# Kernel optimization log

Measured on AMD Instinct MI355X. Metric: run time of the kernel, lower is better.

The kernel has to match this reference:

```python
import jax, jax.numpy as jnp
import numpy as np

DIM = 4096
N_HEADS = 32
HEAD_DIM = DIM // N_HEADS  # 128
B = 2
S = 2048
ADAPTER_LEN = 10
NEG_INF = -1e30


def _rope(t, cos, sin):
    # t: [B, S, H, hd]; cos/sin: [S, hd//2]
    b, s, h, d = t.shape
    tr = t.reshape(b, s, h, d // 2, 2)
    a, bb = tr[..., 0], tr[..., 1]
    c = cos[None, :, None, :]
    sn = sin[None, :, None, :]
    out = jnp.stack([a * c - bb * sn, a * sn + bb * c], axis=-1)
    return out.reshape(b, s, h, d)


def _attn(q, k, v, mask=None):
    # q: [B,H,Q,d], k/v: [B,H,K,d]
    scores = jnp.einsum('bhqd,bhkd->bhqk', q, k) / np.sqrt(HEAD_DIM).astype(q.dtype)
    if mask is not None:
        scores = scores + mask
    probs = jax.nn.softmax(scores.astype(jnp.float32), axis=-1).astype(q.dtype)
    return jnp.einsum('bhqk,bhkd->bhqd', probs, v)


def setup_inputs() -> dict:
    key = jax.random.key(0)
    ks = jax.random.split(key, 8)
    w_std = 0.02
    x = jax.random.normal(ks[0], (B, S, DIM), dtype=jnp.float32)
    wq = jax.random.normal(ks[1], (DIM, DIM), dtype=jnp.float32) * w_std
    wk = jax.random.normal(ks[2], (DIM, DIM), dtype=jnp.float32) * w_std
    wv = jax.random.normal(ks[3], (DIM, DIM), dtype=jnp.float32) * w_std
    wo = jax.random.normal(ks[4], (DIM, DIM), dtype=jnp.float32) * w_std
    gate = jax.random.normal(ks[5], (1, N_HEADS, 1, 1), dtype=jnp.float32)
    adapter = jax.random.normal(ks[6], (1, ADAPTER_LEN, DIM), dtype=jnp.float32)
    # RoPE tables (theta = 10000)
    inv_freq = 1.0 / (10000.0 ** (np.arange(0, HEAD_DIM, 2, dtype=np.float32) / HEAD_DIM))
    angles = np.outer(np.arange(S, dtype=np.float32), inv_freq)  # [S, hd//2]
    freqs_cos = jnp.asarray(np.cos(angles), dtype=jnp.float32)
    freqs_sin = jnp.asarray(np.sin(angles), dtype=jnp.float32)
    # causal additive mask [1,1,S,S]
    mask = jnp.triu(jnp.full((S, S), NEG_INF, dtype=jnp.float32), k=1)[None, None]
    return {"x": x, "wq": wq, "wk": wk, "wv": wv, "wo": wo, "gate": gate,
            "adapter": adapter, "freqs_cos": freqs_cos, "freqs_sin": freqs_sin,
            "mask": mask, "start_pos": 0}


def reference(x, wq, wk, wv, wo, gate, adapter, freqs_cos, freqs_sin, mask, start_pos):
    bsz, seqlen, _ = x.shape
    # QKV projections (torch Linear: y = x @ W.T)
    xq = jnp.einsum('bsd,ed->bse', x, wq).reshape(bsz, seqlen, N_HEADS, HEAD_DIM)
    xk = jnp.einsum('bsd,ed->bse', x, wk).reshape(bsz, seqlen, N_HEADS, HEAD_DIM)
    xv = jnp.einsum('bsd,ed->bse', x, wv).reshape(bsz, seqlen, N_HEADS, HEAD_DIM)
    xq = _rope(xq, freqs_cos, freqs_sin)
    xk = _rope(xk, freqs_cos, freqs_sin)
    # KV-cache write + read: start_pos == 0 and cache is zero-initialized, so
    # keys/values over [:start_pos+seqlen] equal the freshly written xk/xv.
    q = xq.transpose(0, 2, 1, 3)      # [B,H,S,d]
    keys = xk.transpose(0, 2, 1, 3)
    values = xv.transpose(0, 2, 1, 3)
    output = _attn(q, keys, values, mask)
    # gated adapter cross-attention
    a_k = jnp.einsum('bld,ed->ble', adapter, wk).reshape(1, ADAPTER_LEN, N_HEADS, HEAD_DIM)
    a_v = jnp.einsum('bld,ed->ble', adapter, wv).reshape(1, ADAPTER_LEN, N_HEADS, HEAD_DIM)
    a_k = jnp.broadcast_to(a_k, (bsz, ADAPTER_LEN, N_HEADS, HEAD_DIM)).transpose(0, 2, 1, 3)
    a_v = jnp.broadcast_to(a_v, (bsz, ADAPTER_LEN, N_HEADS, HEAD_DIM)).transpose(0, 2, 1, 3)
    output = output + jnp.tanh(gate) * _attn(q, a_k, a_v)
    output = output.transpose(0, 2, 1, 3).reshape(bsz, seqlen, DIM)
    return jnp.einsum('bse,de->bsd', output, wo)
```

## Files before the change

### kernel.cpp

```cpp
#include <hip/hip_runtime.h>

typedef unsigned short u16;
typedef __attribute__((ext_vector_type(8))) short short8;
typedef __attribute__((ext_vector_type(4))) float f32x4;

#define L2E   1.44269504088896340736f
#define SCALE 0.08838834764831845f
#define NEGI  -1e30f
#define WN    ((size_t)4096 * 4096)
#define TNB   ((size_t)2048 * 4096)

__device__ __forceinline__ float b2f(u16 u) {
  union { float f; unsigned int i; } v; v.i = ((unsigned int)u) << 16; return v.f;
}
__device__ __forceinline__ u16 f2b(float f) {
  union { float f; unsigned int i; } v; v.f = f;
  unsigned int r = v.i + 0x7fffu + ((v.i >> 16) & 1u);
  return (u16)(r >> 16);
}
__device__ __forceinline__ void gload16(const u16* g, u16* l) {
  __builtin_amdgcn_global_load_lds((const __attribute__((address_space(1))) void*)g,
                                   (__attribute__((address_space(3))) void*)l, 16, 0, 0);
}
__device__ __forceinline__ short8 ld8_f32_to_bf16(const float* p) {
  float4 a = *(const float4*)p;
  float4 b = *(const float4*)(p + 4);
  short8 pk;
  pk[0] = (short)f2b(a.x); pk[1] = (short)f2b(a.y);
  pk[2] = (short)f2b(a.z); pk[3] = (short)f2b(a.w);
  pk[4] = (short)f2b(b.x); pk[5] = (short)f2b(b.y);
  pk[6] = (short)f2b(b.z); pk[7] = (short)f2b(b.w);
  return pk;
}

__global__ __launch_bounds__(256) void cvt_bf16(const float* __restrict__ src,
                                                u16* __restrict__ dst)
{
  size_t e = ((size_t)blockIdx.x * 256 + threadIdx.x) * 8;
  *(short8*)(dst + e) = ld8_f32_to_bf16(src + e);
}

__global__ __launch_bounds__(256, 2) void gemm_nt(const u16* __restrict__ A,
    const u16* __restrict__ B, void* __restrict__ Cv, int mode)
{
  __shared__ __align__(16) u16 As[128 * 64];
  __shared__ __align__(16) u16 Bs[128 * 64];
  const int tid  = threadIdx.x;
  const int wave = tid >> 6, lane = tid & 63;
  const int quad = lane >> 4, l16 = lane & 15;
  const int bm = blockIdx.y * 128, bn = blockIdx.x * 128;
  const int wm = (wave >> 1) * 64, wn = (wave & 1) * 64;

  f32x4 acc[4][4];
#pragma unroll
  for (int i = 0; i < 4; i++)
#pragma unroll
    for (int j = 0; j < 4; j++) acc[i][j] = (f32x4)0.0f;

  for (int k0 = 0; k0 < 4096; k0 += 64) {
    __syncthreads();
#pragma unroll
    for (int i = 0; i < 4; i++) {
      int c = tid + i * 256;
      int row = c >> 3, cb = (c & 7) << 3;
      gload16(A + (((size_t)(bm + row)) << 12) + k0 + cb, As + c * 8);
      gload16(B + (((size_t)(bn + row)) << 12) + k0 + cb, Bs + c * 8);
    }
    __syncthreads();
#pragma unroll
    for (int ks = 0; ks < 2; ks++) {
      short8 af[4], bf[4];
#pragma unroll
      for (int t = 0; t < 4; t++) {
        af[t] = *(const short8*)(As + (wm + t * 16 + l16) * 64 + ks * 32 + quad * 8);
        bf[t] = *(const short8*)(Bs + (wn + t * 16 + l16) * 64 + ks * 32 + quad * 8);
      }
#pragma unroll
      for (int mt = 0; mt < 4; mt++)
#pragma unroll
        for (int nt = 0; nt < 4; nt++)
          acc[mt][nt] = __builtin_amdgcn_mfma_f32_16x16x32_bf16(af[mt], bf[nt], acc[mt][nt], 0, 0, 0);
    }
  }
#pragma unroll
  for (int mt = 0; mt < 4; mt++)
#pragma unroll
    for (int nt = 0; nt < 4; nt++)
#pragma unroll
      for (int r = 0; r < 4; r++) {
        int row = bm + wm + mt * 16 + quad * 4 + r;
        int col = bn + wn + nt * 16 + l16;
        float v = acc[mt][nt][r];
        if (mode == 2) {
          ((float*)Cv)[(((size_t)row) << 12) + col] = v;
        } else if (mode == 1) {
          ((u16*)Cv)[((size_t)(row >> 11)) * TNB + (((size_t)col) << 11) + (row & 2047)] = f2b(v);
        } else {
          ((u16*)Cv)[(((size_t)row) << 12) + col] = f2b(v);
        }
      }
}

__global__ __launch_bounds__(256) void rope_kernel(u16* __restrict__ Q, u16* __restrict__ K,
    const float* __restrict__ fc, const float* __restrict__ fs)
{
  int gid = blockIdx.x * 256 + threadIdx.x;
  int tsel = gid >> 21;
  int r = gid & 2097151;
  int row = r >> 9, gp = r & 511;
  int s = row & 2047;
  int e0 = gp * 8;
  int i0 = (e0 >> 1) & 63;
  u16* p = (tsel ? K : Q) + (((size_t)row) << 12) + e0;
  short8 v = *(const short8*)p;
  float4 c4 = *(const float4*)(fc + s * 64 + i0);
  float4 s4 = *(const float4*)(fs + s * 64 + i0);
  float cc[4] = {c4.x, c4.y, c4.z, c4.w};
  float ss[4] = {s4.x, s4.y, s4.z, s4.w};
  short8 w;
#pragma unroll
  for (int j = 0; j < 4; j++) {
    float a  = b2f((u16)v[2 * j]);
    float bb = b2f((u16)v[2 * j + 1]);
    w[2 * j]     = (short)f2b(a * cc[j] - bb * ss[j]);
    w[2 * j + 1] = (short)f2b(a * ss[j] + bb * cc[j]);
  }
  *(short8*)p = w;
}

__global__ __launch_bounds__(256) void adapter_kv(const float* __restrict__ adapter,
    const float* __restrict__ wk, const float* __restrict__ wv,
    u16* __restrict__ ak, u16* __restrict__ av)
{
  int gid  = blockIdx.x * 4 + (threadIdx.x >> 6);
  int lane = threadIdx.x & 63;
  int which = (gid >= 40960) ? 1 : 0;
  int rem = gid - which * 40960;
  int l = rem >> 12, col = rem & 4095;
  const float* w = which ? wv : wk;
  u16* o = which ? av : ak;
  const float* arow = adapter + l * 4096;
  const float* wrow = w + (((size_t)col) << 12);
  float sum = 0.f;
#pragma unroll
  for (int i = 0; i < 8; i++) {
    int e = i * 512 + lane * 8;
    float4 a0 = *(const float4*)(arow + e);
    float4 a1 = *(const float4*)(arow + e + 4);
    float4 w0 = *(const float4*)(wrow + e);
    float4 w1 = *(const float4*)(wrow + e + 4);
    sum += a0.x * w0.x + a0.y * w0.y + a0.z * w0.z + a0.w * w0.w
         + a1.x * w1.x + a1.y * w1.y + a1.z * w1.z + a1.w * w1.w;
  }
#pragma unroll
  for (int off = 1; off < 64; off <<= 1) sum += __shfl_xor(sum, off, 64);
  if (lane == 0) o[rem] = f2b(sum);
}

__global__ __launch_bounds__(256, 2) void flash_attn(const u16* __restrict__ Q,
    const u16* __restrict__ K, const u16* __restrict__ V, u16* __restrict__ O)
{
  Q += (size_t)blockIdx.z * TNB;
  K += (size_t)blockIdx.z * TNB;
  V += (size_t)blockIdx.z * TNB;
  O += (size_t)blockIdx.z * TNB;
  __shared__ __align__(16) u16 sm[24576];
  u16* Ks = sm;
  u16* Vs = sm + 8192;
  u16* Ps = sm + 16384;
  const int tid  = threadIdx.x;
  const int wave = tid >> 6, lane = tid & 63;
  const int quad = lane >> 4, l16 = lane & 15;
  const int qt = blockIdx.x;
  const int h  = blockIdx.y;
  const int q0 = qt * 128;
  const size_t qkBase = (size_t)h * 128;
  const size_t vBase  = ((size_t)(h * 128)) << 11;

#pragma unroll
  for (int i = 0; i < 8; i++) {
    int c = tid + i * 256;
    int row = c >> 4, cb = (c & 15) << 3;
    gload16(Q + qkBase + (((size_t)(q0 + row)) << 12) + cb, sm + c * 8);
  }
  __syncthreads();
  short8 qa[2][4];
#pragma unroll
  for (int mt = 0; mt < 2; mt++)
#pragma unroll
    for (int ks = 0; ks < 4; ks++)
      qa[mt][ks] = *(const short8*)(sm + (wave * 32 + mt * 16 + l16) * 128 + ks * 32 + quad * 8);

  f32x4 acc_o[2][8];
#pragma unroll
  for (int mt = 0; mt < 2; mt++)
#pragma unroll
    for (int n = 0; n < 8; n++) acc_o[mt][n] = (f32x4)0.0f;
  float m_st[2][4], l_st[2][4];
#pragma unroll
  for (int mt = 0; mt < 2; mt++)
#pragma unroll
    for (int r = 0; r < 4; r++) { m_st[mt][r] = NEGI; l_st[mt][r] = 0.f; }

  const int qw0 = q0 + wave * 32;
  const int ntiles = 2 * (qt + 1);
  for (int t = 0; t < ntiles; t++) {
    const int kv0 = t * 64;
    __syncthreads();
#pragma unroll
    for (int i = 0; i < 4; i++) {
      int c = tid + i * 256;
      int krow = c >> 4, kcb = (c & 15) << 3;
      gload16(K + qkBase + (((size_t)(kv0 + krow)) << 12) + kcb, Ks + c * 8);
      int vrow = c >> 3, vcb = (c & 7) << 3;
      gload16(V + vBase + (((size_t)vrow) << 11) + kv0 + vcb, Vs + c * 8);
    }
    __syncthreads();

    if (kv0 <= qw0 + 31) {
      f32x4 sc[2][4];
#pragma unroll
      for (int mt = 0; mt < 2; mt++)
#pragma unroll
        for (int nt = 0; nt < 4; nt++) sc[mt][nt] = (f32x4)0.0f;
#pragma unroll
      for (int ks = 0; ks < 4; ks++) {
        short8 kb[4];
#pragma unroll
        for (int nt = 0; nt < 4; nt++)
          kb[nt] = *(const short8*)(Ks + (nt * 16 + l16) * 128 + ks * 32 + quad * 8);
#pragma unroll
        for (int mt = 0; mt < 2; mt++)
#pragma unroll
          for (int nt = 0; nt < 4; nt++)
            sc[mt][nt] = __builtin_amdgcn_mfma_f32_16x16x32_bf16(qa[mt][ks], kb[nt], sc[mt][nt], 0, 0, 0);
      }
#pragma unroll
      for (int mt = 0; mt < 2; mt++)
#pragma unroll
        for (int nt = 0; nt < 4; nt++)
#pragma unroll
          for (int r = 0; r < 4; r++) {
            int qrow = qw0 + mt * 16 + quad * 4 + r;
            int key  = kv0 + nt * 16 + l16;
            float s = sc[mt][nt][r] * SCALE;
            sc[mt][nt][r] = (key > qrow) ? NEGI : s;
          }
      float alpha[2][4];
#pragma unroll
      for (int mt = 0; mt < 2; mt++)
#pragma unroll
        for (int r = 0; r < 4; r++) {
          float mx = fmaxf(fmaxf(sc[mt][0][r], sc[mt][1][r]), fmaxf(sc[mt][2][r], sc[mt][3][r]));
          mx = fmaxf(mx, __shfl_xor(mx, 1, 64));
          mx = fmaxf(mx, __shfl_xor(mx, 2, 64));
          mx = fmaxf(mx, __shfl_xor(mx, 4, 64));
          mx = fmaxf(mx, __shfl_xor(mx, 8, 64));
          float mnew = fmaxf(m_st[mt][r], mx);
          float al = __builtin_amdgcn_exp2f((m_st[mt][r] - mnew) * L2E);
          float rs = 0.f;
#pragma unroll
          for (int nt = 0; nt < 4; nt++) {
            float p = __builtin_amdgcn_exp2f((sc[mt][nt][r] - mnew) * L2E);
            sc[mt][nt][r] = p;
            rs += p;
          }
          rs += __shfl_xor(rs, 1, 64);
          rs += __shfl_xor(rs, 2, 64);
          rs += __shfl_xor(rs, 4, 64);
          rs += __shfl_xor(rs, 8, 64);
          l_st[mt][r] = l_st[mt][r] * al + rs;
          m_st[mt][r] = mnew;
          alpha[mt][r] = al;
        }
#pragma unroll
      for (int mt = 0; mt < 2; mt++)
#pragma unroll
        for (int n = 0; n < 8; n++)
#pragma unroll
          for (int r = 0; r < 4; r++) acc_o[mt][n][r] *= alpha[mt][r];
      u16* Pw = Ps + wave * 2048;
#pragma unroll
      for (int mt = 0; mt < 2; mt++)
#pragma unroll
        for (int nt = 0; nt < 4; nt++)
#pragma unroll
          for (int r = 0; r < 4; r++)
            Pw[(mt * 16 + quad * 4 + r) * 64 + nt * 16 + l16] = f2b(sc[mt][nt][r]);
#pragma unroll
      for (int ks2 = 0; ks2 < 2; ks2++) {
        short8 pa[2];
#pragma unroll
        for (int mt = 0; mt < 2; mt++)
          pa[mt] = *(const short8*)(Pw + (mt * 16 + l16) * 64 + ks2 * 32 + quad * 8);
#pragma unroll
        for (int n = 0; n < 8; n++) {
          short8 vb = *(const short8*)(Vs + (n * 16 + l16) * 64 + ks2 * 32 + quad * 8);
#pragma unroll
          for (int mt = 0; mt < 2; mt++)
            acc_o[mt][n] = __builtin_amdgcn_mfma_f32_16x16x32_bf16(pa[mt], vb, acc_o[mt][n], 0, 0, 0);
        }
      }
    }
  }
#pragma unroll
  for (int mt = 0; mt < 2; mt++)
#pragma unroll
    for (int r = 0; r < 4; r++) {
      float inv = 1.0f / l_st[mt][r];
      int qrow = qw0 + mt * 16 + quad * 4 + r;
#pragma unroll
      for (int n = 0; n < 8; n++) {
        int d = n * 16 + l16;
        O[qkBase + (((size_t)qrow) << 12) + d] = f2b(acc_o[mt][n][r] * inv);
      }
    }
}

__global__ __launch_bounds__(256) void adapter_attn(const u16* __restrict__ Q,
    const u16* __restrict__ ak, const u16* __restrict__ av,
    const float* __restrict__ gate, u16* __restrict__ AO)
{
  int gid  = blockIdx.x * 4 + (threadIdx.x >> 6);
  int lane = threadIdx.x & 63;
  int row = gid >> 5, h = gid & 31;
  float g = tanhf(gate[h]);
  const u16* qp = Q + (((size_t)row) << 12) + h * 128 + lane * 2;
  float qa = b2f(qp[0]), qb = b2f(qp[1]);
  float p[10];
#pragma unroll
  for (int l = 0; l < 10; l++) {
    const u16* kp = ak + l * 4096 + h * 128 + lane * 2;
    p[l] = qa * b2f(kp[0]) + qb * b2f(kp[1]);
  }
#pragma unroll
  for (int l = 0; l < 10; l++)
#pragma unroll
    for (int off = 1; off < 64; off <<= 1) p[l] += __shfl_xor(p[l], off, 64);
  float m = NEGI;
#pragma unroll
  for (int l = 0; l < 10; l++) { p[l] *= SCALE; m = fmaxf(m, p[l]); }
  float sum = 0.f;
#pragma unroll
  for (int l = 0; l < 10; l++) { p[l] = __builtin_amdgcn_exp2f((p[l] - m) * L2E); sum += p[l]; }
  float gi = g / sum;
  float a0 = 0.f, a1 = 0.f;
#pragma unroll
  for (int l = 0; l < 10; l++) {
    const u16* vp = av + l * 4096 + h * 128 + lane * 2;
    a0 += p[l] * b2f(vp[0]);
    a1 += p[l] * b2f(vp[1]);
  }
  u16* op = AO + (((size_t)row) << 12) + h * 128 + lane * 2;
  op[0] = f2b(b2f(op[0]) + gi * a0);
  op[1] = f2b(b2f(op[1]) + gi * a1);
}

extern "C" void kernel_launch(void* const* d_in, const int* in_sizes, int n_in,
                              void* d_out, int out_size, void* d_ws, size_t ws_size,
                              hipStream_t stream) {
  (void)in_sizes; (void)n_in; (void)out_size; (void)ws_size;
  const float* x       = (const float*)d_in[0];
  const float* wq      = (const float*)d_in[1];
  const float* wk      = (const float*)d_in[2];
  const float* wv      = (const float*)d_in[3];
  const float* wo      = (const float*)d_in[4];
  const float* gate    = (const float*)d_in[5];
  const float* adapter = (const float*)d_in[6];
  const float* fc      = (const float*)d_in[7];
  const float* fs      = (const float*)d_in[8];
  float* out = (float*)d_out;

  u16* wb  = (u16*)d_ws;
  u16* xb  = wb + WN;
  u16* Qf  = xb + WN;
  u16* Kf  = Qf + WN;
  u16* Vtf = Kf + WN;
  u16* AOf = xb;
  u16* ak  = Vtf + WN;
  u16* av  = ak + 40960;

  adapter_kv<<<20480, 256, 0, stream>>>(adapter, wk, wv, ak, av);
  cvt_bf16<<<8192, 256, 0, stream>>>(x, xb);

  cvt_bf16<<<8192, 256, 0, stream>>>(wq, wb);
  gemm_nt<<<dim3(32, 32), 256, 0, stream>>>(xb, wb, Qf, 0);
  cvt_bf16<<<8192, 256, 0, stream>>>(wk, wb);
  gemm_nt<<<dim3(32, 32), 256, 0, stream>>>(xb, wb, Kf, 0);
  cvt_bf16<<<8192, 256, 0, stream>>>(wv, wb);
  gemm_nt<<<dim3(32, 32), 256, 0, stream>>>(xb, wb, Vtf, 1);

  rope_kernel<<<16384, 256, 0, stream>>>(Qf, Kf, fc, fs);
  flash_attn<<<dim3(16, 32, 2), 256, 0, stream>>>(Qf, Kf, Vtf, AOf);
  adapter_attn<<<32768, 256, 0, stream>>>(Qf, ak, av, gate, AOf);

  cvt_bf16<<<8192, 256, 0, stream>>>(wo, wb);
  gemm_nt<<<dim3(32, 32), 256, 0, stream>>>(AOf, wb, out, 2);
}
```

Measured before the change: 1.733 ms.

## Swizzle flash-attention LDS tiles, raise MFMA priority, transpose V projection GEMM

```diff
diff --git a/kernel.cpp b/kernel.cpp
--- a/kernel.cpp
+++ b/kernel.cpp
@@ -94,7 +94,7 @@
         if (mode == 2) {
           ((float*)Cv)[(((size_t)row) << 12) + col] = v;
         } else if (mode == 1) {
-          ((u16*)Cv)[((size_t)(row >> 11)) * TNB + (((size_t)col) << 11) + (row & 2047)] = f2b(v);
+          ((u16*)Cv)[((size_t)(col >> 11)) * TNB + (((size_t)row) << 11) + (col & 2047)] = f2b(v);
         } else {
           ((u16*)Cv)[(((size_t)row) << 12) + col] = f2b(v);
         }
@@ -180,7 +180,8 @@
 #pragma unroll
   for (int i = 0; i < 8; i++) {
     int c = tid + i * 256;
-    int row = c >> 4, cb = (c & 15) << 3;
+    int row = c >> 4;
+    int cb  = ((c & 15) ^ (row & 7)) << 3;
     gload16(Q + qkBase + (((size_t)(q0 + row)) << 12) + cb, sm + c * 8);
   }
   __syncthreads();
@@ -188,8 +189,10 @@
 #pragma unroll
   for (int mt = 0; mt < 2; mt++)
 #pragma unroll
-    for (int ks = 0; ks < 4; ks++)
-      qa[mt][ks] = *(const short8*)(sm + (wave * 32 + mt * 16 + l16) * 128 + ks * 32 + quad * 8);
+    for (int ks = 0; ks < 4; ks++) {
+      int qr = wave * 32 + mt * 16 + l16;
+      qa[mt][ks] = *(const short8*)(sm + qr * 128 + (((ks * 4 + quad) ^ (qr & 7)) << 3));
+    }
 
   f32x4 acc_o[2][8];
 #pragma unroll
@@ -210,9 +213,11 @@
 #pragma unroll
     for (int i = 0; i < 4; i++) {
       int c = tid + i * 256;
-      int krow = c >> 4, kcb = (c & 15) << 3;
+      int krow = c >> 4;
+      int kcb  = ((c & 15) ^ (krow & 7)) << 3;
       gload16(K + qkBase + (((size_t)(kv0 + krow)) << 12) + kcb, Ks + c * 8);
-      int vrow = c >> 3, vcb = (c & 7) << 3;
+      int vrow = c >> 3;
+      int vcb  = ((c & 7) ^ (vrow & 7)) << 3;
       gload16(V + vBase + (((size_t)vrow) << 11) + kv0 + vcb, Vs + c * 8);
     }
     __syncthreads();
@@ -223,18 +228,22 @@
       for (int mt = 0; mt < 2; mt++)
 #pragma unroll
         for (int nt = 0; nt < 4; nt++) sc[mt][nt] = (f32x4)0.0f;
+      __builtin_amdgcn_s_setprio(1);
 #pragma unroll
       for (int ks = 0; ks < 4; ks++) {
         short8 kb[4];
 #pragma unroll
-        for (int nt = 0; nt < 4; nt++)
-          kb[nt] = *(const short8*)(Ks + (nt * 16 + l16) * 128 + ks * 32 + quad * 8);
+        for (int nt = 0; nt < 4; nt++) {
+          int kr = nt * 16 + l16;
+          kb[nt] = *(const short8*)(Ks + kr * 128 + (((ks * 4 + quad) ^ (kr & 7)) << 3));
+        }
 #pragma unroll
         for (int mt = 0; mt < 2; mt++)
 #pragma unroll
           for (int nt = 0; nt < 4; nt++)
             sc[mt][nt] = __builtin_amdgcn_mfma_f32_16x16x32_bf16(qa[mt][ks], kb[nt], sc[mt][nt], 0, 0, 0);
       }
+      __builtin_amdgcn_s_setprio(0);
 #pragma unroll
       for (int mt = 0; mt < 2; mt++)
 #pragma unroll
@@ -285,22 +294,30 @@
 #pragma unroll
         for (int nt = 0; nt < 4; nt++)
 #pragma unroll
-          for (int r = 0; r < 4; r++)
-            Pw[(mt * 16 + quad * 4 + r) * 64 + nt * 16 + l16] = f2b(sc[mt][nt][r]);
+          for (int r = 0; r < 4; r++) {
+            int prow = mt * 16 + quad * 4 + r;
+            int pcol = nt * 16 + l16;
+            Pw[prow * 64 + (((pcol >> 3) ^ (prow & 7)) << 3) + (pcol & 7)] = f2b(sc[mt][nt][r]);
+          }
+      __builtin_amdgcn_s_setprio(1);
 #pragma unroll
       for (int ks2 = 0; ks2 < 2; ks2++) {
         short8 pa[2];
 #pragma unroll
-        for (int mt = 0; mt < 2; mt++)
-          pa[mt] = *(const short8*)(Pw + (mt * 16 + l16) * 64 + ks2 * 32 + quad * 8);
+        for (int mt = 0; mt < 2; mt++) {
+          int pr = mt * 16 + l16;
+          pa[mt] = *(const short8*)(Pw + pr * 64 + (((ks2 * 4 + quad) ^ (pr & 7)) << 3));
+        }
 #pragma unroll
         for (int n = 0; n < 8; n++) {
-          short8 vb = *(const short8*)(Vs + (n * 16 + l16) * 64 + ks2 * 32 + quad * 8);
+          int vr = n * 16 + l16;
+          short8 vb = *(const short8*)(Vs + vr * 64 + (((ks2 * 4 + quad) ^ (vr & 7)) << 3));
 #pragma unroll
           for (int mt = 0; mt < 2; mt++)
             acc_o[mt][n] = __builtin_amdgcn_mfma_f32_16x16x32_bf16(pa[mt], vb, acc_o[mt][n], 0, 0, 0);
         }
       }
+      __builtin_amdgcn_s_setprio(0);
     }
   }
 #pragma unroll
@@ -388,7 +405,7 @@
   cvt_bf16<<<8192, 256, 0, stream>>>(wk, wb);
   gemm_nt<<<dim3(32, 32), 256, 0, stream>>>(xb, wb, Kf, 0);
   cvt_bf16<<<8192, 256, 0, stream>>>(wv, wb);
-  gemm_nt<<<dim3(32, 32), 256, 0, stream>>>(xb, wb, Vtf, 1);
+  gemm_nt<<<dim3(32, 32), 256, 0, stream>>>(wb, xb, Vtf, 1);
 
   rope_kernel<<<16384, 256, 0, stream>>>(Qf, Kf, fc, fs);
   flash_attn<<<dim3(16, 32, 2), 256, 0, stream>>>(Qf, Kf, Vtf, AOf);
```

After: 1.612 ms. -7.0%, faster.
